# Optimization experiments

Measured on AMD Instinct MI355X. Metric: run time of the kernel, lower is better.

Reference implementation:

```python
import jax, jax.numpy as jnp
import numpy as np

LN_EPS = 1e-5

def setup_inputs() -> dict:
    key = jax.random.key(0)
    k1, k2, k3, k4 = jax.random.split(key, 4)
    B, N = 4, 4096
    inplanes, planes, loc_planes = 128, 128, 128
    img_fea = jax.random.normal(k1, (B, N, inplanes), dtype=jnp.float32)
    loc_fea = jax.random.normal(k2, (B, N, loc_planes), dtype=jnp.float32)
    # nn.Linear(loc_planes, inplanes*planes): weight (out, in), bias (out,)
    bound = 1.0 / np.sqrt(loc_planes)
    W = jax.random.uniform(k3, (inplanes * planes, loc_planes), minval=-bound, maxval=bound, dtype=jnp.float32)
    b = jax.random.uniform(k4, (inplanes * planes,), minval=-bound, maxval=bound, dtype=jnp.float32)
    gamma = jnp.ones((planes,), dtype=jnp.float32)
    beta = jnp.zeros((planes,), dtype=jnp.float32)
    return {"img_fea": img_fea, "loc_fea": loc_fea, "W": W, "b": b, "gamma": gamma, "beta": beta}

def reference(img_fea, loc_fea, W, b, gamma, beta):
    B, N, _ = loc_fea.shape
    inplanes = img_fea.shape[-1]
    # per-token weight generation: (B,N,loc) @ (loc, in*out) -> (B,N,in,out)
    w = (jnp.einsum('bnc,oc->bno', loc_fea, W) + b)
    planes = w.shape[-1] // inplanes
    w = w.reshape(B, N, inplanes, planes)
    # batched vec-matmul: (B,N,1,in) @ (B,N,in,out) -> (B,N,out)
    y = jnp.einsum('bni,bnio->bno', img_fea, w)
    # LayerNorm over last dim
    mu = jnp.mean(y, axis=-1, keepdims=True)
    var = jnp.mean(jnp.square(y - mu), axis=-1, keepdims=True)
    y = (y - mu) * jax.lax.rsqrt(var + LN_EPS) * gamma + beta
    return jax.nn.relu(y)
```

## Files before the change

kernel.cpp:

```cpp
#include <hip/hip_runtime.h>
#include <stdint.h>

using ushort8 = __attribute__((ext_vector_type(8))) unsigned short;
using bf16x8  = __attribute__((ext_vector_type(8))) __bf16;
using f32x16  = __attribute__((ext_vector_type(16))) float;
using f32x2   = __attribute__((ext_vector_type(2))) float;
using u32x4   = __attribute__((ext_vector_type(4))) uint32_t;
using us4     = __attribute__((ext_vector_type(4))) unsigned short;

__device__ __forceinline__ unsigned short f2bf(float x){
  uint32_t u = __builtin_bit_cast(uint32_t, x);
  u = (u + 0x7FFFu + ((u >> 16) & 1u)) >> 16;
  return (unsigned short)u;
}
__device__ __forceinline__ float bf2f(unsigned short b){
  uint32_t u = ((uint32_t)b) << 16;
  return __builtin_bit_cast(float, u);
}

__device__ __forceinline__ f32x16 mfma16(bf16x8 a, bf16x8 b, f32x16 c){
  return __builtin_amdgcn_mfma_f32_32x32x16_bf16(a, b, c, 0, 0, 0);
}

__device__ __forceinline__ bf16x8 cvt8(const float* p){
  ushort8 v;
  #pragma unroll
  for (int j = 0; j < 8; ++j) v[j] = f2bf(p[j]);
  return __builtin_bit_cast(bf16x8, v);
}

__global__ void prep_wb3(const float* __restrict__ W, const float* __restrict__ bias,
                         unsigned short* __restrict__ Wb3){
  int e = blockIdx.x * 256 + threadIdx.x;
  if (e >= 129 * 16384) return;
  int jj = e & 7, w = (e >> 3) & 7, r = (e >> 6) & 31;
  int ch = (e >> 11) & 1, pt = (e >> 12) & 3, s = e >> 14;
  int p = pt * 32 + r;
  int c = ch * 64 + w * 8 + jj;
  float v = (s < 128) ? W[(s << 14) + (p << 7) + c] : bias[(c << 7) + p];
  Wb3[e] = f2bf(v);
}

__global__ __launch_bounds__(512, 2)
void dynmlp(const float* __restrict__ img, const float* __restrict__ loc,
            const unsigned short* __restrict__ Wb3, float* __restrict__ part){
  __shared__ __align__(16) char smem[66048];
  unsigned short* imgT = (unsigned short*)smem;
  float* ldsY = (float*)smem;

  const int b = blockIdx.x;
  const int tt = b >> 1, h = b & 1;
  const int tid = threadIdx.x, lane = tid & 63, wv = tid >> 6;
  const int pt = wv >> 1, ch = wv & 1;
  const int l31 = lane & 31, lg = lane >> 5;
  const int t0 = tt * 128;

  const char* wslice = (const char*)Wb3 +
      ((size_t)(h * 64) * 8 + (size_t)(pt * 2 + ch)) * 4096 + l31 * 128;
  const char* biasSl = (const char*)Wb3 +
      ((size_t)128 * 8 + (size_t)(pt * 2 + ch)) * 4096 + l31 * 128;

  for (int e = tid; e < 2048; e += 512){
    int tl = e & 127, iq = e >> 7;
    float4 v = *(const float4*)&img[(size_t)(t0 + tl) * 128 + h * 64 + iq * 4];
    int slot = (tl & 31) * 4 + (tl >> 5);
    imgT[(iq * 4 + 0) * 128 + slot] = f2bf(v.x);
    imgT[(iq * 4 + 1) * 128 + slot] = f2bf(v.y);
    imgT[(iq * 4 + 2) * 128 + slot] = f2bf(v.z);
    imgT[(iq * 4 + 3) * 128 + slot] = f2bf(v.w);
  }

  bf16x8 bfr[4][4];
  #pragma unroll
  for (int f = 0; f < 4; ++f){
    int t = t0 + f * 32 + l31;
    #pragma unroll
    for (int cc = 0; cc < 4; ++cc)
      bfr[f][cc] = cvt8(&loc[(size_t)t * 128 + ch * 64 + cc * 16 + lg * 8]);
  }

  f32x16 Z;
  #pragma unroll
  for (int i = 0; i < 16; ++i) Z[i] = 0.0f;
  asm volatile("" : "+v"(Z));

  f32x2 accp[4][8];
  #pragma unroll
  for (int f = 0; f < 4; ++f)
    #pragma unroll
    for (int q = 0; q < 8; ++q) accp[f][q] = (f32x2){0.0f, 0.0f};

  u32x4 avA[4], avB[4];
  {
    const u32x4* g = (const u32x4*)wslice;
    #pragma unroll
    for (int i = 0; i < 4; ++i) avA[i] = g[i * 2 + lg];
  }
  const char* gp = wslice + 32768;

  __syncthreads();

  const unsigned short* imgP = imgT + l31 * 4;

  #define STEPBODY(AV, W4) do { \
    bf16x8 a0 = __builtin_bit_cast(bf16x8, AV[0]); \
    bf16x8 a1 = __builtin_bit_cast(bf16x8, AV[1]); \
    bf16x8 a2 = __builtin_bit_cast(bf16x8, AV[2]); \
    bf16x8 a3 = __builtin_bit_cast(bf16x8, AV[3]); \
    __builtin_amdgcn_s_setprio(1); \
    f32x16 T0 = mfma16(a0, bfr[0][0], Z); \
    f32x16 T1 = mfma16(a0, bfr[1][0], Z); \
    f32x16 T2 = mfma16(a0, bfr[2][0], Z); \
    f32x16 T3 = mfma16(a0, bfr[3][0], Z); \
    T0 = mfma16(a1, bfr[0][1], T0); T1 = mfma16(a1, bfr[1][1], T1); \
    T2 = mfma16(a1, bfr[2][1], T2); T3 = mfma16(a1, bfr[3][1], T3); \
    T0 = mfma16(a2, bfr[0][2], T0); T1 = mfma16(a2, bfr[1][2], T1); \
    T2 = mfma16(a2, bfr[2][2], T2); T3 = mfma16(a2, bfr[3][2], T3); \
    T0 = mfma16(a3, bfr[0][3], T0); T1 = mfma16(a3, bfr[1][3], T1); \
    T2 = mfma16(a3, bfr[2][3], T2); T3 = mfma16(a3, bfr[3][3], T3); \
    __builtin_amdgcn_s_setprio(0); \
    float s0 = bf2f(W4[0]), s1 = bf2f(W4[1]), s2 = bf2f(W4[2]), s3 = bf2f(W4[3]); \
    f32x2 v0 = {s0, s0}, v1 = {s1, s1}, v2 = {s2, s2}, v3 = {s3, s3}; \
    _Pragma("unroll") \
    for (int q = 0; q < 8; ++q){ \
      f32x2 p0 = {T0[2*q], T0[2*q+1]}; \
      f32x2 p1 = {T1[2*q], T1[2*q+1]}; \
      f32x2 p2 = {T2[2*q], T2[2*q+1]}; \
      f32x2 p3 = {T3[2*q], T3[2*q+1]}; \
      asm("v_pk_fma_f32 %0, %1, %2, %0" : "+v"(accp[0][q]) : "v"(p0), "v"(v0)); \
      asm("v_pk_fma_f32 %0, %1, %2, %0" : "+v"(accp[1][q]) : "v"(p1), "v"(v1)); \
      asm("v_pk_fma_f32 %0, %1, %2, %0" : "+v"(accp[2][q]) : "v"(p2), "v"(v2)); \
      asm("v_pk_fma_f32 %0, %1, %2, %0" : "+v"(accp[3][q]) : "v"(p3), "v"(v3)); \
    } \
  } while (0)

  for (int k = 0; k < 64; k += 2){
    us4 w0 = *(const us4*)(imgP + k * 128);
    {
      const u32x4* g = (const u32x4*)gp;
      #pragma unroll
      for (int i = 0; i < 4; ++i) avB[i] = g[i * 2 + lg];
      gp += 32768;
    }
    STEPBODY(avA, w0);

    us4 w1 = *(const us4*)(imgP + (k + 1) * 128);
    if (k + 2 < 64){
      const u32x4* g = (const u32x4*)gp;
      #pragma unroll
      for (int i = 0; i < 4; ++i) avA[i] = g[i * 2 + lg];
      gp += 32768;
    } else if (h == 0){
      const u32x4* g = (const u32x4*)biasSl;
      #pragma unroll
      for (int i = 0; i < 4; ++i) avA[i] = g[i * 2 + lg];
    }
    STEPBODY(avB, w1);
  }

  if (h == 0){
    bf16x8 a0 = __builtin_bit_cast(bf16x8, avA[0]);
    bf16x8 a1 = __builtin_bit_cast(bf16x8, avA[1]);
    bf16x8 a2 = __builtin_bit_cast(bf16x8, avA[2]);
    bf16x8 a3 = __builtin_bit_cast(bf16x8, avA[3]);
    #pragma unroll
    for (int f = 0; f < 4; ++f){
      size_t tr = (size_t)(t0 + f * 32 + l31) * 128 + ch * 64 + lg * 8;
      f32x16 T = mfma16(a0, cvt8(&img[tr]),      Z);
      T = mfma16(a1, cvt8(&img[tr + 16]), T);
      T = mfma16(a2, cvt8(&img[tr + 32]), T);
      T = mfma16(a3, cvt8(&img[tr + 48]), T);
      #pragma unroll
      for (int q = 0; q < 8; ++q){
        accp[f][q][0] += T[2*q];
        accp[f][q][1] += T[2*q+1];
      }
    }
  }

  __syncthreads();
  if (ch == 0){
    #pragma unroll
    for (int f = 0; f < 4; ++f){
      int t_l = f * 32 + l31;
      #pragma unroll
      for (int r = 0; r < 16; ++r){
        int p = pt * 32 + (r & 3) + 8 * (r >> 2) + 4 * lg;
        ldsY[t_l * 129 + p] = accp[f][r >> 1][r & 1];
      }
    }
  }
  __syncthreads();
  if (ch == 1){
    #pragma unroll
    for (int f = 0; f < 4; ++f){
      int t_l = f * 32 + l31;
      #pragma unroll
      for (int r = 0; r < 16; ++r){
        int p = pt * 32 + (r & 3) + 8 * (r >> 2) + 4 * lg;
        ldsY[t_l * 129 + p] += accp[f][r >> 1][r & 1];
      }
    }
  }
  __syncthreads();
  float* dst = part + ((size_t)h * 16384 + t0) * 128;
  #pragma unroll
  for (int k = 0; k < 8; ++k){
    int idx4 = k * 512 + tid;
    int t_l = idx4 >> 5, q = idx4 & 31;
    const float* s = &ldsY[t_l * 129 + q * 4];
    float4 v = {s[0], s[1], s[2], s[3]};
    *(float4*)&dst[t_l * 128 + q * 4] = v;
  }
}

__global__ __launch_bounds__(512)
void lnk(const float* __restrict__ part, const float* __restrict__ gamma,
         const float* __restrict__ beta, float* __restrict__ out){
  const int tid = threadIdx.x, lane = tid & 63, wv = tid >> 6;
  const float* p0 = part;
  const float* p1 = part + (size_t)16384 * 128;
  float g0  = gamma[lane], g1 = gamma[lane + 64];
  float be0 = beta[lane],  be1 = beta[lane + 64];
  int tb = blockIdx.x * 64 + wv * 8;
  #pragma unroll 1
  for (int k = 0; k < 8; ++k){
    size_t t = tb + k;
    float y0 = p0[t * 128 + lane]      + p1[t * 128 + lane];
    float y1 = p0[t * 128 + 64 + lane] + p1[t * 128 + 64 + lane];
    float s = y0 + y1, sq = y0 * y0 + y1 * y1;
    #pragma unroll
    for (int m = 32; m >= 1; m >>= 1){
      s  += __shfl_xor(s, m, 64);
      sq += __shfl_xor(sq, m, 64);
    }
    float mean = s * (1.0f / 128.0f);
    float var  = sq * (1.0f / 128.0f) - mean * mean;
    float rs   = rsqrtf(var + 1e-5f);
    float o0 = fmaxf((y0 - mean) * rs * g0 + be0, 0.0f);
    float o1 = fmaxf((y1 - mean) * rs * g1 + be1, 0.0f);
    out[t * 128 + lane]      = o0;
    out[t * 128 + 64 + lane] = o1;
  }
}

extern "C" void kernel_launch(void* const* d_in, const int* in_sizes, int n_in,
                              void* d_out, int out_size, void* d_ws, size_t ws_size,
                              hipStream_t stream){
  const float* img   = (const float*)d_in[0];
  const float* loc   = (const float*)d_in[1];
  const float* W     = (const float*)d_in[2];
  const float* bias  = (const float*)d_in[3];
  const float* gamma = (const float*)d_in[4];
  const float* beta  = (const float*)d_in[5];
  float* out = (float*)d_out;
  unsigned short* Wb3 = (unsigned short*)d_ws;
  float* part = (float*)((char*)d_ws + 4227072);

  prep_wb3<<<8256, 256, 0, stream>>>(W, bias, Wb3);
  dynmlp<<<256, 512, 0, stream>>>(img, loc, Wb3, part);
  lnk<<<256, 512, 0, stream>>>(part, gamma, beta, out);
}
```

Before: 109.3 us.

## Deepen weight prefetch to four stages and make per-lane weight loads contiguous

Reorders the preprocessed bf16 weight layout so each lane reads 16 contiguous bytes at lane-strided offsets, giving fully coalesced 1KB wavefront loads per fragment. Replaces the two-buffer register prefetch with a four-buffer rotation, so each weight fragment is requested three steps before it is used. The aim is to hide global-memory latency behind the MFMA work. The cost is 32 extra VGPRs per thread under a 2-blocks-per-CU launch bound, which could push register pressure into spills.

```diff
diff --git a/kernel.cpp b/kernel.cpp
--- a/kernel.cpp
+++ b/kernel.cpp
@@ -29,21 +29,22 @@
   return __builtin_bit_cast(bf16x8, v);
 }
 
-__global__ void prep_wb3(const float* __restrict__ W, const float* __restrict__ bias,
-                         unsigned short* __restrict__ Wb3){
+__global__ void prep_wb4(const float* __restrict__ W, const float* __restrict__ bias,
+                         unsigned short* __restrict__ Wb4){
   int e = blockIdx.x * 256 + threadIdx.x;
   if (e >= 129 * 16384) return;
-  int jj = e & 7, w = (e >> 3) & 7, r = (e >> 6) & 31;
-  int ch = (e >> 11) & 1, pt = (e >> 12) & 3, s = e >> 14;
-  int p = pt * 32 + r;
-  int c = ch * 64 + w * 8 + jj;
+  int jj = e & 7, q = (e >> 3) & 255, sl = (e >> 11) & 7, s = e >> 14;
+  int ch = sl & 1, pt = sl >> 1;
+  int cc = q >> 6, lg = (q >> 5) & 1, l31 = q & 31;
+  int p = pt * 32 + l31;
+  int c = ch * 64 + cc * 16 + lg * 8 + jj;
   float v = (s < 128) ? W[(s << 14) + (p << 7) + c] : bias[(c << 7) + p];
-  Wb3[e] = f2bf(v);
+  Wb4[e] = f2bf(v);
 }
 
 __global__ __launch_bounds__(512, 2)
 void dynmlp(const float* __restrict__ img, const float* __restrict__ loc,
-            const unsigned short* __restrict__ Wb3, float* __restrict__ part){
+            const unsigned short* __restrict__ Wb4, float* __restrict__ part){
   __shared__ __align__(16) char smem[66048];
   unsigned short* imgT = (unsigned short*)smem;
   float* ldsY = (float*)smem;
@@ -55,10 +56,10 @@
   const int l31 = lane & 31, lg = lane >> 5;
   const int t0 = tt * 128;
 
-  const char* wslice = (const char*)Wb3 +
-      ((size_t)(h * 64) * 8 + (size_t)(pt * 2 + ch)) * 4096 + l31 * 128;
-  const char* biasSl = (const char*)Wb3 +
-      ((size_t)128 * 8 + (size_t)(pt * 2 + ch)) * 4096 + l31 * 128;
+  const char* wlane = (const char*)Wb4 +
+      ((size_t)(h * 64) * 8 + (size_t)(pt * 2 + ch)) * 4096 + (lane << 4);
+  const char* blane = (const char*)Wb4 +
+      ((size_t)128 * 8 + (size_t)(pt * 2 + ch)) * 4096 + (lane << 4);
 
   for (int e = tid; e < 2048; e += 512){
     int tl = e & 127, iq = e >> 7;
@@ -90,13 +91,12 @@
     #pragma unroll
     for (int q = 0; q < 8; ++q) accp[f][q] = (f32x2){0.0f, 0.0f};
 
-  u32x4 avA[4], avB[4];
-  {
-    const u32x4* g = (const u32x4*)wslice;
-    #pragma unroll
-    for (int i = 0; i < 4; ++i) avA[i] = g[i * 2 + lg];
-  }
-  const char* gp = wslice + 32768;
+  u32x4 b0[4], b1[4], b2[4], b3[4];
+  #define LOADB(BK, STEP) do { \
+    const u32x4* _g = (const u32x4*)(wlane + (size_t)(STEP) * 32768); \
+    BK[0] = _g[0]; BK[1] = _g[64]; BK[2] = _g[128]; BK[3] = _g[192]; \
+  } while (0)
+  LOADB(b0, 0); LOADB(b1, 1); LOADB(b2, 2); LOADB(b3, 3);
 
   __syncthreads();
 
@@ -134,35 +134,37 @@
     } \
   } while (0)
 
-  for (int k = 0; k < 64; k += 2){
-    us4 w0 = *(const us4*)(imgP + k * 128);
-    {
-      const u32x4* g = (const u32x4*)gp;
-      #pragma unroll
-      for (int i = 0; i < 4; ++i) avB[i] = g[i * 2 + lg];
-      gp += 32768;
-    }
-    STEPBODY(avA, w0);
-
-    us4 w1 = *(const us4*)(imgP + (k + 1) * 128);
-    if (k + 2 < 64){
-      const u32x4* g = (const u32x4*)gp;
-      #pragma unroll
-      for (int i = 0; i < 4; ++i) avA[i] = g[i * 2 + lg];
-      gp += 32768;
-    } else if (h == 0){
-      const u32x4* g = (const u32x4*)biasSl;
-      #pragma unroll
-      for (int i = 0; i < 4; ++i) avA[i] = g[i * 2 + lg];
-    }
-    STEPBODY(avB, w1);
+  for (int k = 0; k < 56; k += 4){
+    us4 w;
+    w = *(const us4*)(imgP + (k + 0) * 128); STEPBODY(b0, w); LOADB(b0, k + 4);
+    w = *(const us4*)(imgP + (k + 1) * 128); STEPBODY(b1, w); LOADB(b1, k + 5);
+    w = *(const us4*)(imgP + (k + 2) * 128); STEPBODY(b2, w); LOADB(b2, k + 6);
+    w = *(const us4*)(imgP + (k + 3) * 128); STEPBODY(b3, w); LOADB(b3, k + 7);
+  }
+  {
+    us4 w;
+    w = *(const us4*)(imgP + 56 * 128); STEPBODY(b0, w); LOADB(b0, 60);
+    w = *(const us4*)(imgP + 57 * 128); STEPBODY(b1, w); LOADB(b1, 61);
+    w = *(const us4*)(imgP + 58 * 128); STEPBODY(b2, w); LOADB(b2, 62);
+    w = *(const us4*)(imgP + 59 * 128); STEPBODY(b3, w); LOADB(b3, 63);
+  }
+  {
+    us4 w;
+    w = *(const us4*)(imgP + 60 * 128); STEPBODY(b0, w);
+    if (h == 0){
+      const u32x4* _g = (const u32x4*)blane;
+      b0[0] = _g[0]; b0[1] = _g[64]; b0[2] = _g[128]; b0[3] = _g[192];
+    }
+    w = *(const us4*)(imgP + 61 * 128); STEPBODY(b1, w);
+    w = *(const us4*)(imgP + 62 * 128); STEPBODY(b2, w);
+    w = *(const us4*)(imgP + 63 * 128); STEPBODY(b3, w);
   }
 
   if (h == 0){
-    bf16x8 a0 = __builtin_bit_cast(bf16x8, avA[0]);
-    bf16x8 a1 = __builtin_bit_cast(bf16x8, avA[1]);
-    bf16x8 a2 = __builtin_bit_cast(bf16x8, avA[2]);
-    bf16x8 a3 = __builtin_bit_cast(bf16x8, avA[3]);
+    bf16x8 a0 = __builtin_bit_cast(bf16x8, b0[0]);
+    bf16x8 a1 = __builtin_bit_cast(bf16x8, b0[1]);
+    bf16x8 a2 = __builtin_bit_cast(bf16x8, b0[2]);
+    bf16x8 a3 = __builtin_bit_cast(bf16x8, b0[3]);
     #pragma unroll
     for (int f = 0; f < 4; ++f){
       size_t tr = (size_t)(t0 + f * 32 + l31) * 128 + ch * 64 + lg * 8;
@@ -254,10 +256,10 @@
   const float* gamma = (const float*)d_in[4];
   const float* beta  = (const float*)d_in[5];
   float* out = (float*)d_out;
-  unsigned short* Wb3 = (unsigned short*)d_ws;
+  unsigned short* Wb4 = (unsigned short*)d_ws;
   float* part = (float*)((char*)d_ws + 4227072);
 
-  prep_wb3<<<8256, 256, 0, stream>>>(W, bias, Wb3);
-  dynmlp<<<256, 512, 0, stream>>>(img, loc, Wb3, part);
+  prep_wb4<<<8256, 256, 0, stream>>>(W, bias, Wb4);
+  dynmlp<<<256, 512, 0, stream>>>(img, loc, Wb4, part);
   lnk<<<256, 512, 0, stream>>>(part, gamma, beta, out);
 }
```

After: 184.1 us. 68.5% more time.
